# Kernel optimization log

Measured on AMD Instinct MI355X. Metric: run time of the kernel, lower is better.

The kernel has to match this reference:

```python
import jax, jax.numpy as jnp
import numpy as np

D = 384      # d_model
H = 12       # num_heads
DK = 32      # head dim
L = 6        # num_layers
FF = 1536    # FFN intermediate (4*d_model)
EPS = 1e-12  # BERT LayerNorm eps


def layer_norm(x, w, b):
    m = jnp.mean(x, -1, keepdims=True)
    v = jnp.mean((x - m) ** 2, -1, keepdims=True)
    return (x - m) * jax.lax.rsqrt(v + EPS) * w + b


def deltanet(x, mask, Wq, bq, Wk, bk, Wv, bv, Wb, bb, Wg, bg, Wo, bo, fl, sl):
    # Hierarchical delta-rule linear attention with fast/slow decay states.
    B, S, _ = x.shape
    q = (x @ Wq + bq).reshape(B, S, H, DK)
    k = (x @ Wk + bk).reshape(B, S, H, DK)
    k = k / (jnp.linalg.norm(k, axis=-1, keepdims=True) + 1e-6)
    v = (x @ Wv + bv).reshape(B, S, H, DK)
    beta = jax.nn.sigmoid(x @ Wb + bb) * mask[:, :, None]   # [B,S,H] write gate
    g = jax.nn.sigmoid(x @ Wg + bg)                          # [B,S,H] flux mix gate
    af = jax.nn.sigmoid(fl)[None, :, None, None]             # fast decay, init 0.3
    as_ = jax.nn.sigmoid(sl)[None, :, None, None]            # slow decay, init 0.85

    def step(carry, inp):
        Sf, Ss = carry                      # [B,H,DK,DK] states
        qt, kt, vt, bt, gt = inp            # [B,H,DK],[B,H,DK],[B,H,DK],[B,H],[B,H]
        rf = jnp.einsum('bhkd,bhk->bhd', Sf, kt)
        Sf = af * Sf + bt[..., None, None] * kt[..., :, None] * (vt - rf)[:, :, None, :]
        of = jnp.einsum('bhkd,bhk->bhd', Sf, qt)
        rs = jnp.einsum('bhkd,bhk->bhd', Ss, kt)
        Ss = as_ * Ss + bt[..., None, None] * kt[..., :, None] * (vt - rs)[:, :, None, :]
        os_ = jnp.einsum('bhkd,bhk->bhd', Ss, qt)
        out = gt[..., None] * of + (1.0 - gt[..., None]) * os_
        return (Sf, Ss), out

    to_t = lambda a: jnp.moveaxis(a, 1, 0)  # [B,S,...] -> [S,B,...]
    S0 = jnp.zeros((B, H, DK, DK), x.dtype)
    _, out = jax.lax.scan(step, (S0, S0), (to_t(q), to_t(k), to_t(v), to_t(beta), to_t(g)))
    out = jnp.moveaxis(out, 0, 1).reshape(B, S, D)
    return out @ Wo + bo


def _forward(input_ids, attention_mask, word_emb, pos_emb, type_emb, emb_ln_w, emb_ln_b,
             Wq, bq, Wk, bk, Wv, bv, Wbeta, bbeta, Wg, bg, Wo, bo, fast_logit, slow_logit,
             attn_ln_w, attn_ln_b, ffn_w1, ffn_b1, ffn_w2, ffn_b2, ffn_ln_w, ffn_ln_b):
    B, S = input_ids.shape
    mask = attention_mask.astype(jnp.float32)
    x = word_emb[input_ids] + pos_emb[:S][None] + type_emb[0][None, None]
    x = layer_norm(x, emb_ln_w, emb_ln_b)
    for i in range(L):
        res = x
        a = deltanet(x, mask, Wq[i], bq[i], Wk[i], bk[i], Wv[i], bv[i],
                     Wbeta[i], bbeta[i], Wg[i], bg[i], Wo[i], bo[i],
                     fast_logit[i], slow_logit[i])
        x = layer_norm(res + a, attn_ln_w[i], attn_ln_b[i])
        res = x
        h = jax.nn.gelu(x @ ffn_w1[i] + ffn_b1[i], approximate=False)
        x = layer_norm(res + h @ ffn_w2[i] + ffn_b2[i], ffn_ln_w[i], ffn_ln_b[i])
    m = mask[:, :, None]
    emb = jnp.sum(x * m, 1) / jnp.clip(jnp.sum(m, 1), 1e-9)
    return emb / jnp.linalg.norm(emb, axis=1, keepdims=True)


def setup_inputs() -> dict:
    key = jax.random.key(0)
    ks = jax.random.split(key, 16)
    B, S, V, P = 64, 512, 30522, 512
    n = lambda k, shp, s=0.02: jax.random.normal(k, shp, jnp.float32) * s
    return {
        'input_ids': jax.random.randint(ks[0], (B, S), 0, V),
        'attention_mask': jnp.ones((B, S), jnp.int32),
        'word_emb': n(ks[1], (V, D)),
        'pos_emb': n(ks[2], (P, D)),
        'type_emb': n(ks[3], (2, D)),
        'emb_ln_w': jnp.ones((D,)), 'emb_ln_b': jnp.zeros((D,)),
        'Wq': n(ks[4], (L, D, D)), 'bq': jnp.zeros((L, D)),
        'Wk': n(ks[5], (L, D, D)), 'bk': jnp.zeros((L, D)),
        'Wv': n(ks[6], (L, D, D)), 'bv': jnp.zeros((L, D)),
        'Wbeta': n(ks[7], (L, D, H)), 'bbeta': jnp.zeros((L, H)),
        'Wg': n(ks[8], (L, D, H)), 'bg': jnp.zeros((L, H)),
        'Wo': n(ks[9], (L, D, D)), 'bo': jnp.zeros((L, D)),
        'fast_logit': jnp.full((L, H), -0.8473, jnp.float32),  # sigmoid -> 0.3
        'slow_logit': jnp.full((L, H), 1.7346, jnp.float32),   # sigmoid -> 0.85
        'attn_ln_w': jnp.ones((L, D)), 'attn_ln_b': jnp.zeros((L, D)),
        'ffn_w1': n(ks[10], (L, D, FF)), 'ffn_b1': jnp.zeros((L, FF)),
        'ffn_w2': n(ks[11], (L, FF, D)), 'ffn_b2': jnp.zeros((L, D)),
        'ffn_ln_w': jnp.ones((L, D)), 'ffn_ln_b': jnp.zeros((L, D)),
    }


def reference(input_ids, attention_mask, word_emb, pos_emb, type_emb, emb_ln_w, emb_ln_b,
              Wq, bq, Wk, bk, Wv, bv, Wbeta, bbeta, Wg, bg, Wo, bo, fast_logit, slow_logit,
              attn_ln_w, attn_ln_b, ffn_w1, ffn_b1, ffn_w2, ffn_b2, ffn_ln_w, ffn_ln_b):
    return _forward(input_ids, attention_mask, word_emb, pos_emb, type_emb, emb_ln_w, emb_ln_b,
                    Wq, bq, Wk, bk, Wv, bv, Wbeta, bbeta, Wg, bg, Wo, bo, fast_logit, slow_logit,
                    attn_ln_w, attn_ln_b, ffn_w1, ffn_b1, ffn_w2, ffn_b2, ffn_ln_w, ffn_ln_b)
```

## Files before the change

kernel.cpp:

```cpp
#include <hip/hip_runtime.h>
#include <math.h>

#define DD 384
#define HH 12
#define DKK 32
#define LL 6
#define FFF 1536
#define BB 64
#define SS 512
#define MROWS (BB*SS)
#define TB 32
#define LDX 1152

typedef _Float16 f16;
typedef _Float16 half8 __attribute__((ext_vector_type(8)));
typedef _Float16 h2 __attribute__((ext_vector_type(2)));
typedef float f32x4 __attribute__((ext_vector_type(4)));
typedef float f32x2 __attribute__((ext_vector_type(2)));

__device__ __forceinline__ float sigmoidf_(float x){ return 1.0f/(1.0f+expf(-x)); }

__device__ __forceinline__ float h2f_lo(unsigned int u){
  union { unsigned short s; f16 h; } c; c.s = (unsigned short)(u & 0xffffu); return (float)c.h;
}
__device__ __forceinline__ float h2f_hi(unsigned int u){
  union { unsigned short s; f16 h; } c; c.s = (unsigned short)(u >> 16); return (float)c.h;
}

__device__ __forceinline__ void gl2lds16(const void* g, void* l){
  __builtin_amdgcn_global_load_lds((const __attribute__((address_space(1))) void*)g,
                                   (__attribute__((address_space(3))) void*)l, 16, 0, 0);
}

__device__ __forceinline__ void betag_tail(
    const float* Ws, const float o[6], int lane, int row,
    const float* __restrict__ bbq, const float* __restrict__ bgq,
    const int* __restrict__ mask, float* __restrict__ beta, float* __restrict__ g)
{
  float accb[12], accg[12];
  #pragma unroll
  for (int j=0;j<12;j++){ accb[j]=0.f; accg[j]=0.f; }
  #pragma unroll
  for (int i=0;i<6;i++){
    int k = lane + 64*i;
    float xv = o[i];
    const float* wr = &Ws[k*25];
    #pragma unroll
    for (int j=0;j<12;j++){ accb[j] += xv*wr[j]; accg[j] += xv*wr[12+j]; }
  }
  #pragma unroll
  for (int j=0;j<12;j++){
    #pragma unroll
    for (int off=32; off>=1; off>>=1){
      accb[j]+=__shfl_xor(accb[j],off);
      accg[j]+=__shfl_xor(accg[j],off);
    }
  }
  if (lane==0){
    float mk = (float)mask[row];
    #pragma unroll
    for (int j=0;j<12;j++){
      beta[(size_t)row*HH + j] = sigmoidf_(accb[j]+bbq[j]) * mk;
      g[(size_t)row*HH + j]    = sigmoidf_(accg[j]+bgq[j]);
    }
  }
}

__device__ __forceinline__ void betag_stage(
    float* Ws, const float* __restrict__ Wbp, const float* __restrict__ Wgp)
{
  for (int idx = threadIdx.x; idx < 384*12; idx += 256){
    int k = idx/12, j = idx - k*12;
    Ws[k*25+j]    = Wbp[idx];
    Ws[k*25+12+j] = Wgp[idx];
  }
  __syncthreads();
}

__global__ __launch_bounds__(256) void embed_ln_kernel(
    const int* __restrict__ ids, const float* __restrict__ we,
    const float* __restrict__ pe, const float* __restrict__ te,
    const float* __restrict__ w, const float* __restrict__ b,
    float* __restrict__ x, f16* __restrict__ xh,
    const float* __restrict__ Wbp, const float* __restrict__ bbq,
    const float* __restrict__ Wgp, const float* __restrict__ bgq,
    const int* __restrict__ mask, float* __restrict__ beta, float* __restrict__ g)
{
  extern __shared__ float Ws[];
  betag_stage(Ws, Wbp, Wgp);
  int wv = threadIdx.x >> 6, lane = threadIdx.x & 63;
  int row = blockIdx.x * 4 + wv;
  int s = row & (SS-1);
  int id = ids[row];
  const float* wep = we + (size_t)id * DD;
  const float* pep = pe + (size_t)s * DD;
  float vals[6]; float sum = 0.f;
  #pragma unroll
  for (int i=0;i<6;i++){ int d = lane + 64*i; vals[i] = wep[d] + pep[d] + te[d]; sum += vals[i]; }
  #pragma unroll
  for (int off=32; off>=1; off>>=1) sum += __shfl_xor(sum, off);
  float mean = sum * (1.0f/DD);
  float vs = 0.f;
  #pragma unroll
  for (int i=0;i<6;i++){ float dv = vals[i]-mean; vs += dv*dv; }
  #pragma unroll
  for (int off=32; off>=1; off>>=1) vs += __shfl_xor(vs, off);
  float inv = rsqrtf(vs*(1.0f/DD) + 1e-12f);
  float* xr = x + (size_t)row*DD;
  f16* xhr = xh + (size_t)row*DD;
  #pragma unroll
  for (int i=0;i<6;i++){ int d = lane + 64*i; float o = (vals[i]-mean)*inv*w[d] + b[d]; xr[d]=o; xhr[d]=(f16)o; vals[i]=o; }
  betag_tail(Ws, vals, lane, row, bbq, bgq, mask, beta, g);
}

template<int YH, int BG, int WX>
__global__ __launch_bounds__(256) void add_ln_kernel(
    float* __restrict__ x, f16* __restrict__ xh, const void* __restrict__ yp,
    const float* __restrict__ w, const float* __restrict__ b, int row0, int ldy,
    const float* __restrict__ Wbp, const float* __restrict__ bbq,
    const float* __restrict__ Wgp, const float* __restrict__ bgq,
    const int* __restrict__ mask, float* __restrict__ beta, float* __restrict__ g)
{
  extern __shared__ float Ws[];
  if (BG) betag_stage(Ws, Wbp, Wgp);
  int wv = threadIdx.x >> 6, lane = threadIdx.x & 63;
  int rrel = blockIdx.x * 4 + wv;
  int row = row0 + rrel;
  float* xr = x + (size_t)row*DD;
  f16* xhr = xh + (size_t)row*DD;
  float vals[6]; float sum = 0.f;
  #pragma unroll
  for (int i=0;i<6;i++){
    int d = lane + 64*i;
    float yv;
    if (YH) yv = (float)((const f16*)yp)[(size_t)rrel*ldy + d];
    else    yv = ((const float*)yp)[(size_t)rrel*ldy + d];
    vals[i] = xr[d] + yv; sum += vals[i];
  }
  #pragma unroll
  for (int off=32; off>=1; off>>=1) sum += __shfl_xor(sum, off);
  float mean = sum * (1.0f/DD);
  float vs = 0.f;
  #pragma unroll
  for (int i=0;i<6;i++){ float dv = vals[i]-mean; vs += dv*dv; }
  #pragma unroll
  for (int off=32; off>=1; off>>=1) vs += __shfl_xor(vs, off);
  float inv = rsqrtf(vs*(1.0f/DD) + 1e-12f);
  #pragma unroll
  for (int i=0;i<6;i++){
    int d = lane + 64*i;
    float o = (vals[i]-mean)*inv*w[d] + b[d];
    xr[d]=o;
    if (WX) xhr[d]=(f16)o;
    vals[i]=o;
  }
  if (BG) betag_tail(Ws, vals, lane, row, bbq, bgq, mask, beta, g);
}

__global__ __launch_bounds__(256) void biaspack_kernel(
    const float* __restrict__ bq, const float* __restrict__ bk, const float* __restrict__ bv,
    float* __restrict__ dst)
{
  int i = blockIdx.x*256 + threadIdx.x;
  if (i >= LL*LDX) return;
  int l = i / LDX, r = i - l*LDX;
  float v;
  if (r < 384) v = bq[l*DD + r];
  else if (r < 768) v = bk[l*DD + r-384];
  else v = bv[l*DD + r-768];
  dst[i] = v;
}

__global__ __launch_bounds__(256) void wtrans_kernel(
  const float* __restrict__ Wq, const float* __restrict__ Wk, const float* __restrict__ Wv,
  const float* __restrict__ Wo, const float* __restrict__ W1, const float* __restrict__ W2,
  f16* __restrict__ Wt)
{
  __shared__ float T[32][33];
  int l = blockIdx.x / 1728, bidx = blockIdx.x % 1728;
  const float* src; f16* dst; int K, N, tile;
  if (bidx < 576){ int m = bidx/144; tile = bidx - m*144; K=384; N=384;
    const float* w4[4] = {Wq + (size_t)l*147456, Wk + (size_t)l*147456,
                          Wv + (size_t)l*147456, Wo + (size_t)l*147456};
    src = w4[m]; dst = Wt + (size_t)l*1769472 + m*147456; }
  else if (bidx < 1152){ tile = bidx-576; K=384; N=1536;
    src = W1 + (size_t)l*589824; dst = Wt + (size_t)l*1769472 + 589824; }
  else { tile = bidx-1152; K=1536; N=384;
    src = W2 + (size_t)l*589824; dst = Wt + (size_t)l*1769472 + 1179648; }
  int tN = N>>5;
  int tk = tile / tN, tn = tile - tk*tN;
  int k0 = tk<<5, n0 = tn<<5;
  int r = threadIdx.x >> 3, c4 = (threadIdx.x & 7) << 2;
  float4 vv = *(const float4*)(src + (size_t)(k0+r)*N + n0 + c4);
  T[r][c4+0]=vv.x; T[r][c4+1]=vv.y; T[r][c4+2]=vv.z; T[r][c4+3]=vv.w;
  __syncthreads();
  f16* dp = dst + (size_t)(n0+r)*K + k0 + c4;
  #pragma unroll
  for (int j=0;j<4;j++) dp[j] = (f16)T[c4+j][r];
}

template<int ACT, int OUT16>
__global__ __launch_bounds__(256) void gemm_f16(
    const f16* __restrict__ A, const f16* __restrict__ BT,
    const float* __restrict__ bias, float* __restrict__ Cf, f16* __restrict__ Ch,
    int M, int N, int K, int lda, int ldc)
{
  __shared__ __align__(16) f16 As[2][2][128*32];
  __shared__ __align__(16) f16 Bs[2][2][128*32];
  int tid = threadIdx.x, lane = tid & 63, wave = tid >> 6;
  int wm = wave >> 1, wn = wave & 1;
  int gx = gridDim.x, gy = gridDim.y;
  int bid = blockIdx.y * gx + blockIdx.x;
  int chunk = (gx * gy) >> 3;
  int nf = (bid & 7) * chunk + (bid >> 3);
  int ty = nf / gx, tx = nf - ty * gx;
  int n0 = tx * 128, m0 = ty * 128;
  f32x4 acc[4][4] = {};
  int seg0 = wave*2048 + lane*16;
  int ar = lane & 15, kq = (lane >> 4) * 8;

  #define GSTAGE(PB, K0) do {                                                  \
    _Pragma("unroll")                                                          \
    for (int i=0;i<2;i++){                                                     \
      int seg = seg0 + i*1024;                                                 \
      int e = seg >> 1; int row = e >> 5; int kk = e & 31;                     \
      const f16* ap = A  + (size_t)(m0+row)*lda + (K0) + kk;                   \
      const f16* bp = BT + (size_t)(n0+row)*K   + (K0) + kk;                   \
      gl2lds16(ap,      (char*)As[PB][0] + seg);                               \
      gl2lds16(ap + 32, (char*)As[PB][1] + seg);                               \
      gl2lds16(bp,      (char*)Bs[PB][0] + seg);                               \
      gl2lds16(bp + 32, (char*)Bs[PB][1] + seg);                               \
    }                                                                          \
  } while(0)

  GSTAGE(0, 0);
  __syncthreads();
  int nk = K >> 6;
  int pb = 0;
  for (int t=0; t<nk; t++){
    if (t+1 < nk) GSTAGE(pb^1, (t+1)*64);
    #pragma unroll
    for (int h=0; h<2; h++){
      half8 af[4], bfr[4];
      #pragma unroll
      for (int mi=0;mi<4;mi++) af[mi]  = *(const half8*)&As[pb][h][(wm*64 + mi*16 + ar)*32 + kq];
      #pragma unroll
      for (int ni=0;ni<4;ni++) bfr[ni] = *(const half8*)&Bs[pb][h][(wn*64 + ni*16 + ar)*32 + kq];
      #pragma unroll
      for (int mi=0;mi<4;mi++)
        #pragma unroll
        for (int ni=0;ni<4;ni++)
          acc[mi][ni] = __builtin_amdgcn_mfma_f32_16x16x32_f16(af[mi], bfr[ni], acc[mi][ni], 0, 0, 0);
    }
    __syncthreads();
    pb ^= 1;
  }
  #undef GSTAGE

  int rb = (lane >> 4) * 4, cb = lane & 15;
  #pragma unroll
  for (int ni=0;ni<4;ni++){
    int cn = n0 + wn*64 + ni*16 + cb;
    float bz = bias[cn];
    #pragma unroll
    for (int mi=0;mi<4;mi++){
      int rm = m0 + wm*64 + mi*16 + rb;
      #pragma unroll
      for (int r=0;r<4;r++){
        float v = acc[mi][ni][r] + bz;
        if (ACT==1) v = 0.5f*v*(1.0f+erff(v*0.70710678118f));
        if (OUT16) Ch[(size_t)(rm+r)*ldc + cn] = (f16)v;
        else       Cf[(size_t)(rm+r)*ldc + cn] = v;
      }
    }
  }
}

__global__ __launch_bounds__(64) void scan_kernel(
  f16* qkv,
  const float* __restrict__ bp, const float* __restrict__ gp,
  const float* __restrict__ flp, const float* __restrict__ slp)
{
  __shared__ float Kf[2][TB][32];
  __shared__ float Qf[2][TB][32];
  __shared__ float Vf[2][TB][32];
  __shared__ float Bg[2][2][TB];
  __shared__ float Of[TB][64];
  int blk = blockIdx.x;
  int b = blk / HH, h = blk - b*HH;
  int lane = threadIdx.x;
  int col = lane & 31;
  float a = sigmoidf_((lane < 32) ? flp[h] : slp[h]);
  f32x2 a2 = {a, a};
  f32x2 S2[16];
  #pragma unroll
  for (int j=0;j<16;j++) S2[j] = (f32x2){0.f,0.f};
  size_t base = ((size_t)b*SS)*LDX + (size_t)h*DKK;
  f16* qb = qkv + base;
  const f16* kb = qkv + base + 384;
  const f16* vb = qkv + base + 768;
  const float* bbp = bp + ((size_t)b*SS)*HH + h;
  const float* gbp = gp + ((size_t)b*SS)*HH + h;

  int st0 = lane >> 2, part = lane & 3;
  uint4 kv[2], qv[2], vv[2]; float bgv;

  #define LOADG(T0) do {                                                       \
    _Pragma("unroll")                                                          \
    for (int r=0;r<2;r++){                                                     \
      int st = (T0) + r*16 + st0;                                              \
      size_t off = (size_t)st*LDX + part*8;                                    \
      kv[r] = *(const uint4*)(kb + off);                                       \
      qv[r] = *(const uint4*)(qb + off);                                       \
      vv[r] = *(const uint4*)(vb + off);                                       \
    }                                                                          \
    int tb_ = (T0) + (lane & 31);                                              \
    bgv = (lane < 32) ? bbp[(size_t)tb_*HH] : gbp[(size_t)tb_*HH];             \
  } while(0)

  #define STAGE(BUF) do {                                                      \
    _Pragma("unroll")                                                          \
    for (int r=0;r<2;r++){                                                     \
      int s = r*16 + st0;                                                      \
      float kf[8], qf[8], vf[8];                                               \
      kf[0]=h2f_lo(kv[r].x); kf[1]=h2f_hi(kv[r].x); kf[2]=h2f_lo(kv[r].y);     \
      kf[3]=h2f_hi(kv[r].y); kf[4]=h2f_lo(kv[r].z); kf[5]=h2f_hi(kv[r].z);     \
      kf[6]=h2f_lo(kv[r].w); kf[7]=h2f_hi(kv[r].w);                            \
      qf[0]=h2f_lo(qv[r].x); qf[1]=h2f_hi(qv[r].x); qf[2]=h2f_lo(qv[r].y);     \
      qf[3]=h2f_hi(qv[r].y); qf[4]=h2f_lo(qv[r].z); qf[5]=h2f_hi(qv[r].z);     \
      qf[6]=h2f_lo(qv[r].w); qf[7]=h2f_hi(qv[r].w);                            \
      vf[0]=h2f_lo(vv[r].x); vf[1]=h2f_hi(vv[r].x); vf[2]=h2f_lo(vv[r].y);     \
      vf[3]=h2f_hi(vv[r].y); vf[4]=h2f_lo(vv[r].z); vf[5]=h2f_hi(vv[r].z);     \
      vf[6]=h2f_lo(vv[r].w); vf[7]=h2f_hi(vv[r].w);                            \
      float ss = 0.f;                                                          \
      _Pragma("unroll")                                                        \
      for (int i=0;i<8;i++) ss += kf[i]*kf[i];                                 \
      ss += __shfl_xor(ss, 1); ss += __shfl_xor(ss, 2);                        \
      float sc = 1.0f/(sqrtf(ss)+1e-6f);                                       \
      float4 t;                                                                \
      t.x=kf[0]*sc; t.y=kf[1]*sc; t.z=kf[2]*sc; t.w=kf[3]*sc;                  \
      *(float4*)&Kf[BUF][s][part*8] = t;                                       \
      t.x=kf[4]*sc; t.y=kf[5]*sc; t.z=kf[6]*sc; t.w=kf[7]*sc;                  \
      *(float4*)&Kf[BUF][s][part*8+4] = t;                                     \
      t.x=qf[0]; t.y=qf[1]; t.z=qf[2]; t.w=qf[3];                              \
      *(float4*)&Qf[BUF][s][part*8] = t;                                       \
      t.x=qf[4]; t.y=qf[5]; t.z=qf[6]; t.w=qf[7];                              \
      *(float4*)&Qf[BUF][s][part*8+4] = t;                                     \
      t.x=vf[0]; t.y=vf[1]; t.z=vf[2]; t.w=vf[3];                              \
      *(float4*)&Vf[BUF][s][part*8] = t;                                       \
      t.x=vf[4]; t.y=vf[5]; t.z=vf[6]; t.w=vf[7];                              \
      *(float4*)&Vf[BUF][s][part*8+4] = t;                                     \
    }                                                                          \
    Bg[BUF][lane>>5][lane&31] = bgv;                                           \
  } while(0)

  #define LDSTEP(BUF,S,KR,QR,VT,BT) do {                                       \
    const float4* k4_ = (const float4*)&Kf[BUF][S][0];                         \
    const float4* q4_ = (const float4*)&Qf[BUF][S][0];                         \
    _Pragma("unroll")                                                          \
    for (int j=0;j<8;j++){ KR[j]=k4_[j]; QR[j]=q4_[j]; }                       \
    VT = Vf[BUF][S][col]; BT = Bg[BUF][0][S];                                  \
  } while(0)

  #define STEP(KR,QR,VT,BT,S) do {                                            \
    const f32x2* k2_ = (const f32x2*)KR;                                       \
    const f32x2* q2_ = (const f32x2*)QR;                                       \
    f32x2 rA={0.f,0.f},rB={0.f,0.f},rC={0.f,0.f},rD={0.f,0.f};                 \
    _Pragma("unroll")                                                          \
    for (int j=0;j<16;j+=4){                                                   \
      rA += S2[j+0]*k2_[j+0]; rB += S2[j+1]*k2_[j+1];                          \
      rC += S2[j+2]*k2_[j+2]; rD += S2[j+3]*k2_[j+3]; }                        \
    f32x2 rr = (rA+rB)+(rC+rD);                                                \
    float rf = rr.x + rr.y;                                                    \
    float c_ = (BT)*((VT) - rf);                                               \
    f32x2 c2 = {c_, c_};                                                       \
    _Pragma("unroll")                                                          \
    for (int j=0;j<16;j++) S2[j] = a2*S2[j] + c2*k2_[j];                       \
    f32x2 oA={0.f,0.f},oB={0.f,0.f},oC={0.f,0.f},oD={0.f,0.f};                 \
    _Pragma("unroll")                                                          \
    for (int j=0;j<16;j+=4){                                                   \
      oA += S2[j+0]*q2_[j+0]; oB += S2[j+1]*q2_[j+1];                          \
      oC += S2[j+2]*q2_[j+2]; oD += S2[j+3]*q2_[j+3]; }                        \
    f32x2 oo = (oA+oB)+(oC+oD);                                                \
    Of[S][lane] = oo.x + oo.y;                                                 \
  } while(0)

  #define COMBINE(BUF,T0) do {                                                 \
    _Pragma("unroll")                                                          \
    for (int i=0;i<16;i++){                                                    \
      int idx = i*64 + lane;                                                   \
      int s_ = idx >> 5, c_ = idx & 31;                                        \
      float fv = Of[s_][c_];                                                   \
      float sv = Of[s_][c_+32];                                                \
      float gv = Bg[BUF][1][s_];                                               \
      qb[(size_t)((T0)+s_)*LDX + c_] = (f16)(gv*fv + (1.0f-gv)*sv);            \
    }                                                                          \
  } while(0)

  LOADG(0);
  STAGE(0);
  __syncthreads();

  float4 kA[8], qA[8], kB[8], qB[8];
  float vA, bA, vB, bB;

  for (int tile=0; tile<SS/TB; tile++){
    int buf = tile & 1;
    if (tile < SS/TB-1) LOADG((tile+1)*TB);
    LDSTEP(buf, 0, kA, qA, vA, bA);
    #pragma unroll
    for (int s=0; s<TB; s+=2){
      if (s+1 < TB) LDSTEP(buf, s+1, kB, qB, vB, bB);
      STEP(kA, qA, vA, bA, s);
      if (s+2 < TB) LDSTEP(buf, s+2, kA, qA, vA, bA);
      STEP(kB, qB, vB, bB, s+1);
    }
    if (tile < SS/TB-1) STAGE(1-buf);
    COMBINE(buf, tile*TB);
    __syncthreads();
  }
  #undef LOADG
  #undef STAGE
  #undef LDSTEP
  #undef STEP
  #undef COMBINE
}

__global__ __launch_bounds__(384) void pool_kernel(
    const float* __restrict__ x, const int* __restrict__ mask, float* __restrict__ out)
{
  __shared__ float red[384];
  __shared__ float tot;
  int b = blockIdx.x, d = threadIdx.x;
  const float* xb = x + (size_t)b*SS*DD;
  const int* mb = mask + b*SS;
  float s=0.f, sm=0.f;
  for (int t=0;t<SS;t++){ float m=(float)mb[t]; s += xb[(size_t)t*DD+d]*m; sm += m; }
  float emb = s / fmaxf(sm, 1e-9f);
  red[d] = emb*emb;
  __syncthreads();
  for (int off=192; off>=3; off>>=1){
    if (d < off) red[d] += red[d+off];
    __syncthreads();
  }
  if (d==0) tot = red[0]+red[1]+red[2];
  __syncthreads();
  out[(size_t)b*DD + d] = emb * rsqrtf(tot);
}

extern "C" void kernel_launch(void* const* d_in, const int* in_sizes, int n_in,
                              void* d_out, int out_size, void* d_ws, size_t ws_size,
                              hipStream_t stream)
{
  const int*   ids  = (const int*)d_in[0];
  const int*   amask= (const int*)d_in[1];
  const float* we   = (const float*)d_in[2];
  const float* pe   = (const float*)d_in[3];
  const float* te   = (const float*)d_in[4];
  const float* elnw = (const float*)d_in[5];
  const float* elnb = (const float*)d_in[6];
  const float* Wq   = (const float*)d_in[7];
  const float* bq   = (const float*)d_in[8];
  const float* Wk   = (const float*)d_in[9];
  const float* bk   = (const float*)d_in[10];
  const float* Wv   = (const float*)d_in[11];
  const float* bv   = (const float*)d_in[12];
  const float* Wb   = (const float*)d_in[13];
  const float* bb   = (const float*)d_in[14];
  const float* Wg   = (const float*)d_in[15];
  const float* bgp  = (const float*)d_in[16];
  const float* Wo   = (const float*)d_in[17];
  const float* bo   = (const float*)d_in[18];
  const float* fl   = (const float*)d_in[19];
  const float* sl   = (const float*)d_in[20];
  const float* alnw = (const float*)d_in[21];
  const float* alnb = (const float*)d_in[22];
  const float* W1   = (const float*)d_in[23];
  const float* b1   = (const float*)d_in[24];
  const float* W2   = (const float*)d_in[25];
  const float* b2   = (const float*)d_in[26];
  const float* flnw = (const float*)d_in[27];
  const float* flnb = (const float*)d_in[28];
  float* out = (float*)d_out;
  float* w = (float*)d_ws;

  float* x    = w;
  f16*  xh   = (f16*)(w + 12582912);
  f16*  qkvh = (f16*)(w + 18874368);
  float* f2   = w + 37748736;
  float* beta = f2 + 3145728;
  float* gbuf = beta + 393216;
  f16*  wt   = (f16*)(w + 44040192);
  float* bqkv = w + 49348608;
  f16*  hb   = qkvh;

  const size_t BGLDS = 384*25*sizeof(float);

  embed_ln_kernel<<<MROWS/4, 256, BGLDS, stream>>>(ids, we, pe, te, elnw, elnb, x, xh,
                                                   Wb, bb, Wg, bgp, amask, beta, gbuf);
  biaspack_kernel<<<27,256,0,stream>>>(bq, bk, bv, bqkv);
  wtrans_kernel<<<LL*1728,256,0,stream>>>(Wq, Wk, Wv, Wo, W1, W2, wt);

  for (int l=0;l<LL;l++){
    f16* wl = wt + (size_t)l*1769472;

    gemm_f16<0,1><<<dim3(9,256),256,0,stream>>>(xh, wl, bqkv + l*LDX, nullptr, qkvh,
                                                MROWS, LDX, DD, DD, LDX);

    scan_kernel<<<BB*HH,64,0,stream>>>(qkvh, beta, gbuf, fl + l*HH, sl + l*HH);

    gemm_f16<0,1><<<dim3(3,256),256,0,stream>>>(qkvh, wl+442368, bo+l*DD, nullptr,
                                                qkvh + 384, MROWS, DD, DD, LDX, LDX);
    add_ln_kernel<1,0,1><<<MROWS/4,256,0,stream>>>(x, xh, qkvh + 384, alnw+l*DD, alnb+l*DD, 0, LDX,
                                                   nullptr, nullptr, nullptr, nullptr,
                                                   nullptr, nullptr, nullptr);

    gemm_f16<1,1><<<dim3(12,256),256,0,stream>>>(xh, wl+589824, b1+l*FFF, nullptr, hb,
                                                 MROWS, FFF, DD, DD, FFF);
    gemm_f16<0,1><<<dim3(3,256),256,0,stream>>>(hb, wl+1179648, b2+l*DD, nullptr, xh,
                                                MROWS, DD, FFF, FFF, DD);
    if (l < LL-1)
      add_ln_kernel<1,1,1><<<MROWS/4,256,BGLDS,stream>>>(x, xh, xh, flnw+l*DD, flnb+l*DD, 0, DD,
                                                         Wb + (size_t)(l+1)*DD*HH, bb + (l+1)*HH,
                                                         Wg + (size_t)(l+1)*DD*HH, bgp + (l+1)*HH,
                                                         amask, beta, gbuf);
    else
      add_ln_kernel<1,0,0><<<MROWS/4,256,0,stream>>>(x, xh, xh, flnw+l*DD, flnb+l*DD, 0, DD,
                                                     nullptr, nullptr, nullptr, nullptr,
                                                     nullptr, nullptr, nullptr);
  }

  pool_kernel<<<BB,384,0,stream>>>(x, amask, out);
}
```

Before: 2.992 ms.

## Process two (batch,head) scans per wavefront with interleaved independent recurrences

The scan kernel now handles two independent (batch, head) pairs per 64-thread block, launching half as many blocks. The two recurrences are interleaved step by step to expose instruction-level parallelism and hide the dependent FMA chain latency. The time tile shrinks from 32 to 16 to keep shared memory in check. This doubles register state per thread and halves the number of blocks, which may reduce occupancy and the parallelism across CUs.

New measurement: 3.763 ms. 25.7% more time.

```diff
diff --git a/kernel.cpp b/kernel.cpp
--- a/kernel.cpp
+++ b/kernel.cpp
@@ -9,7 +9,7 @@
 #define BB 64
 #define SS 512
 #define MROWS (BB*SS)
-#define TB 32
+#define TB 16
 #define LDX 1152
 
 typedef _Float16 f16;
@@ -281,80 +281,83 @@
   const float* __restrict__ bp, const float* __restrict__ gp,
   const float* __restrict__ flp, const float* __restrict__ slp)
 {
-  __shared__ float Kf[2][TB][32];
-  __shared__ float Qf[2][TB][32];
-  __shared__ float Vf[2][TB][32];
-  __shared__ float Bg[2][2][TB];
-  __shared__ float Of[TB][64];
+  __shared__ float KfA[2][TB][32], QfA[2][TB][32], VfA[2][TB][32];
+  __shared__ float KfB[2][TB][32], QfB[2][TB][32], VfB[2][TB][32];
+  __shared__ float BgA[2][2][TB], BgB[2][2][TB];
+  __shared__ float OfA[TB][64], OfB[TB][64];
   int blk = blockIdx.x;
-  int b = blk / HH, h = blk - b*HH;
+  int p0 = blk*2, p1 = blk*2+1;
+  int b0 = p0 / HH, h0 = p0 - b0*HH;
+  int b1 = p1 / HH, h1 = p1 - b1*HH;
   int lane = threadIdx.x;
   int col = lane & 31;
-  float a = sigmoidf_((lane < 32) ? flp[h] : slp[h]);
-  f32x2 a2 = {a, a};
-  f32x2 S2[16];
-  #pragma unroll
-  for (int j=0;j<16;j++) S2[j] = (f32x2){0.f,0.f};
-  size_t base = ((size_t)b*SS)*LDX + (size_t)h*DKK;
-  f16* qb = qkv + base;
-  const f16* kb = qkv + base + 384;
-  const f16* vb = qkv + base + 768;
-  const float* bbp = bp + ((size_t)b*SS)*HH + h;
-  const float* gbp = gp + ((size_t)b*SS)*HH + h;
+  float aA = sigmoidf_((lane < 32) ? flp[h0] : slp[h0]);
+  float aB = sigmoidf_((lane < 32) ? flp[h1] : slp[h1]);
+  f32x2 aA2 = {aA, aA}, aB2 = {aB, aB};
+  f32x2 SA[16], SB[16];
+  #pragma unroll
+  for (int j=0;j<16;j++){ SA[j] = (f32x2){0.f,0.f}; SB[j] = (f32x2){0.f,0.f}; }
+  size_t baseA = ((size_t)b0*SS)*LDX + (size_t)h0*DKK;
+  size_t baseB = ((size_t)b1*SS)*LDX + (size_t)h1*DKK;
+  f16* qbA = qkv + baseA;              const f16* kbA = qkv + baseA + 384;
+  const f16* vbA = qkv + baseA + 768;
+  f16* qbB = qkv + baseB;              const f16* kbB = qkv + baseB + 384;
+  const f16* vbB = qkv + baseB + 768;
+  const float* bbpA = bp + ((size_t)b0*SS)*HH + h0;
+  const float* gbpA = gp + ((size_t)b0*SS)*HH + h0;
+  const float* bbpB = bp + ((size_t)b1*SS)*HH + h1;
+  const float* gbpB = gp + ((size_t)b1*SS)*HH + h1;
 
   int st0 = lane >> 2, part = lane & 3;
-  uint4 kv[2], qv[2], vv[2]; float bgv;
+  uint4 kvA, qvA, vvA, kvB, qvB, vvB; float bgvA, bgvB;
 
   #define LOADG(T0) do {                                                       \
-    _Pragma("unroll")                                                          \
-    for (int r=0;r<2;r++){                                                     \
-      int st = (T0) + r*16 + st0;                                              \
-      size_t off = (size_t)st*LDX + part*8;                                    \
-      kv[r] = *(const uint4*)(kb + off);                                       \
-      qv[r] = *(const uint4*)(qb + off);                                       \
-      vv[r] = *(const uint4*)(vb + off);                                       \
-    }                                                                          \
-    int tb_ = (T0) + (lane & 31);                                              \
-    bgv = (lane < 32) ? bbp[(size_t)tb_*HH] : gbp[(size_t)tb_*HH];             \
+    size_t off = (size_t)((T0) + st0)*LDX + part*8;                            \
+    kvA = *(const uint4*)(kbA + off);                                          \
+    qvA = *(const uint4*)(qbA + off);                                          \
+    vvA = *(const uint4*)(vbA + off);                                          \
+    kvB = *(const uint4*)(kbB + off);                                          \
+    qvB = *(const uint4*)(qbB + off);                                          \
+    vvB = *(const uint4*)(vbB + off);                                          \
+    int tb_ = (T0) + (lane & 15);                                              \
+    bgvA = (lane < 32) ? bbpA[(size_t)tb_*HH] : gbpA[(size_t)tb_*HH];          \
+    bgvB = (lane < 32) ? bbpB[(size_t)tb_*HH] : gbpB[(size_t)tb_*HH];          \
   } while(0)
 
-  #define STAGE(BUF) do {                                                      \
-    _Pragma("unroll")                                                          \
-    for (int r=0;r<2;r++){                                                     \
-      int s = r*16 + st0;                                                      \
-      float kf[8], qf[8], vf[8];                                               \
-      kf[0]=h2f_lo(kv[r].x); kf[1]=h2f_hi(kv[r].x); kf[2]=h2f_lo(kv[r].y);     \
-      kf[3]=h2f_hi(kv[r].y); kf[4]=h2f_lo(kv[r].z); kf[5]=h2f_hi(kv[r].z);     \
-      kf[6]=h2f_lo(kv[r].w); kf[7]=h2f_hi(kv[r].w);                            \
-      qf[0]=h2f_lo(qv[r].x); qf[1]=h2f_hi(qv[r].x); qf[2]=h2f_lo(qv[r].y);     \
-      qf[3]=h2f_hi(qv[r].y); qf[4]=h2f_lo(qv[r].z); qf[5]=h2f_hi(qv[r].z);     \
-      qf[6]=h2f_lo(qv[r].w); qf[7]=h2f_hi(qv[r].w);                            \
-      vf[0]=h2f_lo(vv[r].x); vf[1]=h2f_hi(vv[r].x); vf[2]=h2f_lo(vv[r].y);     \
-      vf[3]=h2f_hi(vv[r].y); vf[4]=h2f_lo(vv[r].z); vf[5]=h2f_hi(vv[r].z);     \
-      vf[6]=h2f_lo(vv[r].w); vf[7]=h2f_hi(vv[r].w);                            \
-      float ss = 0.f;                                                          \
-      _Pragma("unroll")                                                        \
-      for (int i=0;i<8;i++) ss += kf[i]*kf[i];                                 \
-      ss += __shfl_xor(ss, 1); ss += __shfl_xor(ss, 2);                        \
-      float sc = 1.0f/(sqrtf(ss)+1e-6f);                                       \
-      float4 t;                                                                \
-      t.x=kf[0]*sc; t.y=kf[1]*sc; t.z=kf[2]*sc; t.w=kf[3]*sc;                  \
-      *(float4*)&Kf[BUF][s][part*8] = t;                                       \
-      t.x=kf[4]*sc; t.y=kf[5]*sc; t.z=kf[6]*sc; t.w=kf[7]*sc;                  \
-      *(float4*)&Kf[BUF][s][part*8+4] = t;                                     \
-      t.x=qf[0]; t.y=qf[1]; t.z=qf[2]; t.w=qf[3];                              \
-      *(float4*)&Qf[BUF][s][part*8] = t;                                       \
-      t.x=qf[4]; t.y=qf[5]; t.z=qf[6]; t.w=qf[7];                              \
-      *(float4*)&Qf[BUF][s][part*8+4] = t;                                     \
-      t.x=vf[0]; t.y=vf[1]; t.z=vf[2]; t.w=vf[3];                              \
-      *(float4*)&Vf[BUF][s][part*8] = t;                                       \
-      t.x=vf[4]; t.y=vf[5]; t.z=vf[6]; t.w=vf[7];                              \
-      *(float4*)&Vf[BUF][s][part*8+4] = t;                                     \
-    }                                                                          \
-    Bg[BUF][lane>>5][lane&31] = bgv;                                           \
+  #define STAGE1(BUF, kv, qv, vv, bgv, Kf, Qf, Vf, Bg) do {                    \
+    int s = st0;                                                               \
+    float kf[8], qf[8], vf[8];                                                 \
+    kf[0]=h2f_lo(kv.x); kf[1]=h2f_hi(kv.x); kf[2]=h2f_lo(kv.y);                \
+    kf[3]=h2f_hi(kv.y); kf[4]=h2f_lo(kv.z); kf[5]=h2f_hi(kv.z);                \
+    kf[6]=h2f_lo(kv.w); kf[7]=h2f_hi(kv.w);                                    \
+    qf[0]=h2f_lo(qv.x); qf[1]=h2f_hi(qv.x); qf[2]=h2f_lo(qv.y);                \
+    qf[3]=h2f_hi(qv.y); qf[4]=h2f_lo(qv.z); qf[5]=h2f_hi(qv.z);                \
+    qf[6]=h2f_lo(qv.w); qf[7]=h2f_hi(qv.w);                                    \
+    vf[0]=h2f_lo(vv.x); vf[1]=h2f_hi(vv.x); vf[2]=h2f_lo(vv.y);                \
+    vf[3]=h2f_hi(vv.y); vf[4]=h2f_lo(vv.z); vf[5]=h2f_hi(vv.z);                \
+    vf[6]=h2f_lo(vv.w); vf[7]=h2f_hi(vv.w);                                    \
+    float ss = 0.f;                                                            \
+    _Pragma("unroll")                                                          \
+    for (int i=0;i<8;i++) ss += kf[i]*kf[i];                                   \
+    ss += __shfl_xor(ss, 1); ss += __shfl_xor(ss, 2);                          \
+    float sc = 1.0f/(sqrtf(ss)+1e-6f);                                         \
+    float4 t;                                                                  \
+    t.x=kf[0]*sc; t.y=kf[1]*sc; t.z=kf[2]*sc; t.w=kf[3]*sc;                    \
+    *(float4*)&Kf[BUF][s][part*8] = t;                                         \
+    t.x=kf[4]*sc; t.y=kf[5]*sc; t.z=kf[6]*sc; t.w=kf[7]*sc;                    \
+    *(float4*)&Kf[BUF][s][part*8+4] = t;                                       \
+    t.x=qf[0]; t.y=qf[1]; t.z=qf[2]; t.w=qf[3];                                \
+    *(float4*)&Qf[BUF][s][part*8] = t;                                         \
+    t.x=qf[4]; t.y=qf[5]; t.z=qf[6]; t.w=qf[7];                                \
+    *(float4*)&Qf[BUF][s][part*8+4] = t;                                       \
+    t.x=vf[0]; t.y=vf[1]; t.z=vf[2]; t.w=vf[3];                                \
+    *(float4*)&Vf[BUF][s][part*8] = t;                                         \
+    t.x=vf[4]; t.y=vf[5]; t.z=vf[6]; t.w=vf[7];                                \
+    *(float4*)&Vf[BUF][s][part*8+4] = t;                                       \
+    Bg[BUF][lane>>5][lane&15] = bgv;                                           \
   } while(0)
 
-  #define LDSTEP(BUF,S,KR,QR,VT,BT) do {                                       \
+  #define LDSTEP1(BUF,S,KR,QR,VT,BT,Kf,Qf,Vf,Bg) do {                          \
     const float4* k4_ = (const float4*)&Kf[BUF][S][0];                         \
     const float4* q4_ = (const float4*)&Qf[BUF][S][0];                         \
     _Pragma("unroll")                                                          \
@@ -362,7 +365,7 @@
     VT = Vf[BUF][S][col]; BT = Bg[BUF][0][S];                                  \
   } while(0)
 
-  #define STEP(KR,QR,VT,BT,S) do {                                            \
+  #define STEP1(KR,QR,VT,BT,S,S2,a2,Of) do {                                   \
     const f32x2* k2_ = (const f32x2*)KR;                                       \
     const f32x2* q2_ = (const f32x2*)QR;                                       \
     f32x2 rA={0.f,0.f},rB={0.f,0.f},rC={0.f,0.f},rD={0.f,0.f};                 \
@@ -385,9 +388,9 @@
     Of[S][lane] = oo.x + oo.y;                                                 \
   } while(0)
 
-  #define COMBINE(BUF,T0) do {                                                 \
-    _Pragma("unroll")                                                          \
-    for (int i=0;i<16;i++){                                                    \
+  #define COMBINE1(BUF,T0,Of,Bg,qb) do {                                       \
+    _Pragma("unroll")                                                          \
+    for (int i=0;i<8;i++){                                                     \
       int idx = i*64 + lane;                                                   \
       int s_ = idx >> 5, c_ = idx & 31;                                        \
       float fv = Of[s_][c_];                                                   \
@@ -398,32 +401,36 @@
   } while(0)
 
   LOADG(0);
-  STAGE(0);
+  STAGE1(0, kvA, qvA, vvA, bgvA, KfA, QfA, VfA, BgA);
+  STAGE1(0, kvB, qvB, vvB, bgvB, KfB, QfB, VfB, BgB);
   __syncthreads();
 
-  float4 kA[8], qA[8], kB[8], qB[8];
+  float4 kRA[8], qRA[8], kRB[8], qRB[8];
   float vA, bA, vB, bB;
 
   for (int tile=0; tile<SS/TB; tile++){
     int buf = tile & 1;
     if (tile < SS/TB-1) LOADG((tile+1)*TB);
-    LDSTEP(buf, 0, kA, qA, vA, bA);
     #pragma unroll
-    for (int s=0; s<TB; s+=2){
-      if (s+1 < TB) LDSTEP(buf, s+1, kB, qB, vB, bB);
-      STEP(kA, qA, vA, bA, s);
-      if (s+2 < TB) LDSTEP(buf, s+2, kA, qA, vA, bA);
-      STEP(kB, qB, vB, bB, s+1);
+    for (int s=0; s<TB; s++){
+      LDSTEP1(buf, s, kRA, qRA, vA, bA, KfA, QfA, VfA, BgA);
+      LDSTEP1(buf, s, kRB, qRB, vB, bB, KfB, QfB, VfB, BgB);
+      STEP1(kRA, qRA, vA, bA, s, SA, aA2, OfA);
+      STEP1(kRB, qRB, vB, bB, s, SB, aB2, OfB);
     }
-    if (tile < SS/TB-1) STAGE(1-buf);
-    COMBINE(buf, tile*TB);
+    if (tile < SS/TB-1){
+      STAGE1(1-buf, kvA, qvA, vvA, bgvA, KfA, QfA, VfA, BgA);
+      STAGE1(1-buf, kvB, qvB, vvB, bgvB, KfB, QfB, VfB, BgB);
+    }
+    COMBINE1(buf, tile*TB, OfA, BgA, qbA);
+    COMBINE1(buf, tile*TB, OfB, BgB, qbB);
     __syncthreads();
   }
   #undef LOADG
-  #undef STAGE
-  #undef LDSTEP
-  #undef STEP
-  #undef COMBINE
+  #undef STAGE1
+  #undef LDSTEP1
+  #undef STEP1
+  #undef COMBINE1
 }
 
 __global__ __launch_bounds__(384) void pool_kernel(
@@ -507,7 +514,7 @@
     gemm_f16<0,1><<<dim3(9,256),256,0,stream>>>(xh, wl, bqkv + l*LDX, nullptr, qkvh,
                                                 MROWS, LDX, DD, DD, LDX);
 
-    scan_kernel<<<BB*HH,64,0,stream>>>(qkvh, beta, gbuf, fl + l*HH, sl + l*HH);
+    scan_kernel<<<BB*HH/2,64,0,stream>>>(qkvh, beta, gbuf, fl + l*HH, sl + l*HH);
 
     gemm_f16<0,1><<<dim3(3,256),256,0,stream>>>(qkvh, wl+442368, bo+l*DD, nullptr,
                                                 qkvh + 384, MROWS, DD, DD, LDX, LDX);
```
